# Optimization experiments

Measured on AMD Instinct MI355X. Metric: run time of the kernel, lower is better.

The kernel has to match this reference:

```python
import jax, jax.numpy as jnp
import numpy as np

N, E = 50000, 800000
IN_F, EDGE_F = 512, 32
HEADS, HID = 4, 64  # per-layer: H*C = 256
NEG_SLOPE = 0.2


def _gatv2_layer(x, src, dst, edge_attr, Wl, bl, Wr, br, We, att, bias):
    # PyG GATv2Conv: x_l = lin_l(x) (used as message value), x_r = lin_r(x)
    n = x.shape[0]
    H, C = att.shape
    xl = (x @ Wl + bl).reshape(n, H, C)
    xr = (x @ Wr + br).reshape(n, H, C)
    ea = (edge_attr @ We).reshape(-1, H, C)          # lin_edge (no bias)
    m = jax.nn.leaky_relu(xl[src] + xr[dst] + ea, NEG_SLOPE)  # [E,H,C]
    logits = jnp.einsum('ehc,hc->eh', m, att)        # [E,H]
    # segment softmax over incoming edges of each destination node
    mx = jax.ops.segment_max(logits, dst, num_segments=n)
    ex = jnp.exp(logits - mx[dst])
    denom = jax.ops.segment_sum(ex, dst, num_segments=n)
    alpha = ex / denom[dst]                          # [E,H]
    out = jax.ops.segment_sum(alpha[:, :, None] * xl[src], dst, num_segments=n)
    return out.reshape(n, H * C) + bias


def setup_inputs() -> dict:
    key = jax.random.key(0)
    ks = jax.random.split(key, 16)
    s = lambda fan_in: 1.0 / np.sqrt(fan_in)
    inp = {
        'x': jax.random.normal(ks[0], (N, IN_F), jnp.float32),
        'edge_index': jax.random.randint(ks[1], (2, E), 0, N, jnp.int64),
        'edge_attr': jax.random.normal(ks[2], (E, EDGE_F), jnp.float32),
        'W_l0': jax.random.normal(ks[3], (IN_F, HEADS * HID), jnp.float32) * s(IN_F),
        'b_l0': jnp.zeros((HEADS * HID,), jnp.float32),
        'W_r0': jax.random.normal(ks[4], (IN_F, HEADS * HID), jnp.float32) * s(IN_F),
        'b_r0': jnp.zeros((HEADS * HID,), jnp.float32),
        'W_e0': jax.random.normal(ks[5], (EDGE_F, HEADS * HID), jnp.float32) * s(EDGE_F),
        'att0': jax.random.normal(ks[6], (HEADS, HID), jnp.float32) * s(HID),
        'bias0': jnp.zeros((HEADS * HID,), jnp.float32),
        'W_l1': jax.random.normal(ks[7], (HEADS * HID, HEADS * HID), jnp.float32) * s(HEADS * HID),
        'b_l1': jnp.zeros((HEADS * HID,), jnp.float32),
        'W_r1': jax.random.normal(ks[8], (HEADS * HID, HEADS * HID), jnp.float32) * s(HEADS * HID),
        'b_r1': jnp.zeros((HEADS * HID,), jnp.float32),
        'W_e1': jax.random.normal(ks[9], (EDGE_F, HEADS * HID), jnp.float32) * s(EDGE_F),
        'att1': jax.random.normal(ks[10], (HEADS, HID), jnp.float32) * s(HID),
        'bias1': jnp.zeros((HEADS * HID,), jnp.float32),
        'W_out': jax.random.normal(ks[11], (HEADS * HID, 1), jnp.float32) * s(HEADS * HID),
        'b_out': jnp.zeros((1,), jnp.float32),
    }
    return inp


def reference(x, edge_index, edge_attr,
              W_l0, b_l0, W_r0, b_r0, W_e0, att0, bias0,
              W_l1, b_l1, W_r1, b_r1, W_e1, att1, bias1,
              W_out, b_out):
    src, dst = edge_index[0], edge_index[1]
    h = jax.nn.relu(_gatv2_layer(x, src, dst, edge_attr, W_l0, b_l0, W_r0, b_r0, W_e0, att0, bias0))
    h = jax.nn.relu(_gatv2_layer(h, src, dst, edge_attr, W_l1, b_l1, W_r1, b_r1, W_e1, att1, bias1))
    return h @ W_out + b_out
```

## Files before the change

kernel.cpp:

```cpp
#include <hip/hip_runtime.h>
#include <hip/hip_bf16.h>

#define NEG_SLOPE 0.2f

typedef __attribute__((ext_vector_type(8))) short bf16x8;
typedef __attribute__((ext_vector_type(4))) float f32x4;

__device__ __forceinline__ unsigned short bf16hi(float v) {
    __hip_bfloat16 h = __float2bfloat16(v);
    return *(unsigned short*)&h;
}
__device__ __forceinline__ float bf16tof(unsigned short u) {
    __hip_bfloat16 h = *(__hip_bfloat16*)&u;
    return __bfloat162float(h);
}

__global__ void hist_kernel(const int* __restrict__ dst, int* __restrict__ cnt, int E) {
    int e = blockIdx.x * 256 + threadIdx.x;
    if (e < E) atomicAdd(&cnt[dst[e]], 1);
}

__global__ void scan_s1(const int* __restrict__ cnt, int* __restrict__ excl,
                        int* __restrict__ totals, int N) {
    __shared__ int lds[256];
    int t = threadIdx.x;
    int i = blockIdx.x * 256 + t;
    int v = (i < N) ? cnt[i] : 0;
    lds[t] = v;
    __syncthreads();
    #pragma unroll
    for (int off = 1; off < 256; off <<= 1) {
        int add = (t >= off) ? lds[t - off] : 0;
        __syncthreads();
        lds[t] += add;
        __syncthreads();
    }
    if (i < N) excl[i] = lds[t] - v;
    if (t == 255) totals[blockIdx.x] = lds[255];
}

__global__ void scan_s2(int* __restrict__ totals, int nb) {
    __shared__ int lds[256];
    int t = threadIdx.x;
    int v = (t < nb) ? totals[t] : 0;
    lds[t] = v;
    __syncthreads();
    #pragma unroll
    for (int off = 1; off < 256; off <<= 1) {
        int add = (t >= off) ? lds[t - off] : 0;
        __syncthreads();
        lds[t] += add;
        __syncthreads();
    }
    if (t < nb) totals[t] = lds[t] - v;
}

__global__ void scan_s3(int* __restrict__ row_ptr, const int* __restrict__ totals,
                        int* __restrict__ cursor, int N, int E) {
    int i = blockIdx.x * 256 + threadIdx.x;
    if (i < N) {
        int v = row_ptr[i] + totals[blockIdx.x];
        row_ptr[i] = v;
        cursor[i] = v;
    }
    if (i == 0) row_ptr[N] = E;
}

__global__ void scatter_kernel(const int* __restrict__ src, const int* __restrict__ dst,
                               int* __restrict__ cursor, int* __restrict__ col_src,
                               int* __restrict__ col_dst, int* __restrict__ col_eid, int E) {
    int e = blockIdx.x * 256 + threadIdx.x;
    if (e < E) {
        int d = dst[e];
        int pos = atomicAdd(&cursor[d], 1);
        col_src[pos] = src[e];
        col_dst[pos] = d;
        col_eid[pos] = e;
    }
}

__global__ void pack_we(const float* __restrict__ We0, const float* __restrict__ We1,
                        unsigned short* __restrict__ WeP) {
    int t = blockIdx.x * 256 + threadIdx.x;
    if (t >= 4096) return;
    int layer = t >> 11;
    int part  = (t >> 10) & 1;
    int tile  = (t >> 6) & 15;
    int lane  = t & 63;
    const float* We = layer ? We1 : We0;
    int ch = tile * 16 + (lane & 15);
    int kb = (lane >> 4) * 8;
    union { unsigned short u[8]; uint4 v; } out;
    #pragma unroll
    for (int j = 0; j < 8; ++j) {
        float w = We[(size_t)(kb + j) * 256 + ch];
        unsigned short hi = bf16hi(w);
        out.u[j] = part ? bf16hi(w - bf16tof(hi)) : hi;
    }
    *(uint4*)(WeP + (size_t)t * 8) = out.v;
}

__global__ void pack_w(const float* __restrict__ Wl, const float* __restrict__ Wr,
                       int KT, unsigned short* __restrict__ out) {
    int t = blockIdx.x * 256 + threadIdx.x;
    int per = KT * 2048;
    if (t >= 2 * per) return;
    int part = t / per;
    int rem  = t % per;
    int kt   = rem >> 11;
    int nt   = (rem >> 6) & 31;
    int lane = rem & 63;
    int n  = nt * 16 + (lane & 15);
    int kb = kt * 32 + ((lane >> 4) * 8);
    const float* W = (n < 256) ? (Wl + n) : (Wr + (n - 256));
    union { unsigned short u[8]; uint4 v; } o;
    #pragma unroll
    for (int j = 0; j < 8; ++j) {
        float w = W[(size_t)(kb + j) * 256];
        unsigned short hi = bf16hi(w);
        o.u[j] = part ? bf16hi(w - bf16tof(hi)) : hi;
    }
    *(uint4*)(out + (size_t)t * 8) = o.v;
}

__global__ __launch_bounds__(256) void gemm_split(
    const float* __restrict__ A, int M, int K,
    const unsigned short* __restrict__ Bf,
    const float* __restrict__ bl, const float* __restrict__ br,
    float* __restrict__ C)
{
    __shared__ unsigned short Af[2][8][64][8];
    const int tid  = threadIdx.x;
    const int lane = tid & 63;
    const int w    = tid >> 6;
    const int m0   = blockIdx.x * 128;
    const int n0   = blockIdx.y * 128;
    const int KT   = K >> 5;
    const int ntg0 = n0 >> 4;

    f32x4 acc[2][8];
    #pragma unroll
    for (int i = 0; i < 2; ++i)
        #pragma unroll
        for (int j = 0; j < 8; ++j) acc[i][j] = (f32x4){0.f, 0.f, 0.f, 0.f};

    const size_t partStride = (size_t)KT * 32 * 512;

    for (int kt = 0; kt < KT; ++kt) {
        #pragma unroll
        for (int i = 0; i < 4; ++i) {
            int idx = tid * 4 + i;
            int r   = idx >> 3;
            int kl  = (idx & 7) * 4;
            int gm  = m0 + r;
            float4 v = make_float4(0.f, 0.f, 0.f, 0.f);
            if (gm < M) v = *(const float4*)(A + (size_t)gm * K + kt * 32 + kl);
            unsigned short h0 = bf16hi(v.x), h1 = bf16hi(v.y);
            unsigned short h2 = bf16hi(v.z), h3 = bf16hi(v.w);
            unsigned short l0 = bf16hi(v.x - bf16tof(h0));
            unsigned short l1 = bf16hi(v.y - bf16tof(h1));
            unsigned short l2 = bf16hi(v.z - bf16tof(h2));
            unsigned short l3 = bf16hi(v.w - bf16tof(h3));
            int mt = r >> 4;
            int la = (r & 15) | ((kl >> 3) << 4);
            int j0 = kl & 7;
            *(uint2*)&Af[0][mt][la][j0] =
                make_uint2((unsigned int)h0 | ((unsigned int)h1 << 16),
                           (unsigned int)h2 | ((unsigned int)h3 << 16));
            *(uint2*)&Af[1][mt][la][j0] =
                make_uint2((unsigned int)l0 | ((unsigned int)l1 << 16),
                           (unsigned int)l2 | ((unsigned int)l3 << 16));
        }
        __syncthreads();

        bf16x8 ah0 = *(const bf16x8*)&Af[0][w * 2 + 0][lane][0];
        bf16x8 ah1 = *(const bf16x8*)&Af[0][w * 2 + 1][lane][0];
        bf16x8 al0 = *(const bf16x8*)&Af[1][w * 2 + 0][lane][0];
        bf16x8 al1 = *(const bf16x8*)&Af[1][w * 2 + 1][lane][0];

        const unsigned short* bbase =
            Bf + ((size_t)kt * 32 + ntg0) * 512 + (size_t)lane * 8;
        #pragma unroll
        for (int nt = 0; nt < 8; ++nt) {
            bf16x8 bh  = *(const bf16x8*)(bbase + (size_t)nt * 512);
            bf16x8 blv = *(const bf16x8*)(bbase + partStride + (size_t)nt * 512);
            acc[0][nt] = __builtin_amdgcn_mfma_f32_16x16x32_bf16(ah0, bh,  acc[0][nt], 0, 0, 0);
            acc[1][nt] = __builtin_amdgcn_mfma_f32_16x16x32_bf16(ah1, bh,  acc[1][nt], 0, 0, 0);
            acc[0][nt] = __builtin_amdgcn_mfma_f32_16x16x32_bf16(ah0, blv, acc[0][nt], 0, 0, 0);
            acc[1][nt] = __builtin_amdgcn_mfma_f32_16x16x32_bf16(ah1, blv, acc[1][nt], 0, 0, 0);
            acc[0][nt] = __builtin_amdgcn_mfma_f32_16x16x32_bf16(al0, bh,  acc[0][nt], 0, 0, 0);
            acc[1][nt] = __builtin_amdgcn_mfma_f32_16x16x32_bf16(al1, bh,  acc[1][nt], 0, 0, 0);
        }
        __syncthreads();
    }

    const int q  = lane >> 4;
    const int cl = lane & 15;
    #pragma unroll
    for (int mti = 0; mti < 2; ++mti) {
        int gmb = m0 + (w * 2 + mti) * 16 + q * 4;
        #pragma unroll
        for (int nt = 0; nt < 8; ++nt) {
            int col = n0 + nt * 16 + cl;
            float bia = (col < 256) ? bl[col] : br[col - 256];
            #pragma unroll
            for (int r = 0; r < 4; ++r) {
                int gm = gmb + r;
                if (gm < M) C[(size_t)gm * 512 + col] = acc[mti][nt][r] + bia;
            }
        }
    }
}

template<bool PROJ>
__global__ __launch_bounds__(256) void gat_fused_t(
    const float* __restrict__ xlxr,
    const float* __restrict__ edge_attr,
    const int* __restrict__ col_src,
    const int* __restrict__ col_dst,
    const int* __restrict__ col_eid,
    const int* __restrict__ row_ptr,
    const unsigned short* __restrict__ WePl,
    const float* __restrict__ att,
    const float* __restrict__ bias,
    float* __restrict__ nmr,
    const float* __restrict__ Wout,
    const float* __restrict__ bout,
    float* __restrict__ out,
    float* __restrict__ denomB,
    int E, int W)
{
    __shared__ unsigned short AhiS[16][64][8];
    __shared__ unsigned short AloS[16][64][8];
    const int tid = threadIdx.x;
    #pragma unroll
    for (int i = 0; i < 4; ++i) {
        int idx = tid * 4 + i;
        ((uint4*)&AhiS[0][0][0])[idx] = ((const uint4*)WePl)[idx];
        ((uint4*)&AloS[0][0][0])[idx] = ((const uint4*)(WePl + 8192))[idx];
    }
    __syncthreads();

    const int lane  = tid & 63;
    const int wid   = tid >> 6;
    const int q     = lane >> 4;
    const int e_sub = lane & 15;
    const int kb    = q * 8;
    const int ch4   = lane * 4;

    const int gw = blockIdx.x * 4 + wid;
    const int s_range = gw * W;
    if (s_range >= E) return;
    const int eEnd = min(E, s_range + W);

    const float4 bia4 = *(const float4*)(bias + ch4);
    float4 wo4 = make_float4(0.f, 0.f, 0.f, 0.f);
    if (PROJ) wo4 = *(const float4*)(Wout + ch4);

    int curDst = -1;
    float4 accB = make_float4(0.f, 0.f, 0.f, 0.f);
    float denB = 0.f;

    auto flush = [&]() {
        if (curDst >= 0) {
            int ra = row_ptr[curDst], rb = row_ptr[curDst + 1];
            bool comp = (ra % W != 0) && (rb % W != 0) && (ra / W == (rb - 1) / W);
            if (comp) {
                float inv = 1.0f / denB;
                float4 o;
                o.x = fmaxf(fmaf(accB.x, inv, bia4.x), 0.f);
                o.y = fmaxf(fmaf(accB.y, inv, bia4.y), 0.f);
                o.z = fmaxf(fmaf(accB.z, inv, bia4.z), 0.f);
                o.w = fmaxf(fmaf(accB.w, inv, bia4.w), 0.f);
                if (!PROJ) {
                    *(float4*)(nmr + (size_t)curDst * 256 + ch4) = o;
                } else {
                    float s = o.x * wo4.x;
                    s = fmaf(o.y, wo4.y, s);
                    s = fmaf(o.z, wo4.z, s);
                    s = fmaf(o.w, wo4.w, s);
                    #pragma unroll
                    for (int off = 32; off > 0; off >>= 1)
                        s += __shfl_xor(s, off, 64);
                    if (lane == 0) out[curDst] = s + bout[0];
                }
            } else {
                float* np = nmr + (size_t)curDst * 256 + ch4;
                atomicAdd(np + 0, accB.x);
                atomicAdd(np + 1, accB.y);
                atomicAdd(np + 2, accB.z);
                atomicAdd(np + 3, accB.w);
                if (e_sub == 0) atomicAdd(denomB + curDst * 4 + q, denB);
            }
            accB = make_float4(0.f, 0.f, 0.f, 0.f);
            denB = 0.f;
        }
    };

    for (int base = s_range; base < eEnd; base += 16) {
        const int cnt  = min(16, eEnd - base);
        const int slot = base + e_sub;
        const int sc   = min(slot, eEnd - 1);
        const int eid  = col_eid[sc];
        const int srcn = col_src[sc];
        const int dstn = col_dst[sc];

        const float* ap = edge_attr + (size_t)eid * 32 + kb;
        float4 v0 = *(const float4*)ap;
        float4 v1 = *(const float4*)(ap + 4);
        float vv[8] = {v0.x, v0.y, v0.z, v0.w, v1.x, v1.y, v1.z, v1.w};
        union { bf16x8 v; unsigned short u[8]; } bh, bl;
        #pragma unroll
        for (int i = 0; i < 8; ++i) {
            unsigned short hh = bf16hi(vv[i]);
            bh.u[i] = hh;
            bl.u[i] = bf16hi(vv[i] - bf16tof(hh));
        }

        const float* xlp = xlxr + (size_t)srcn * 512 + q * 4;
        const float* xrp = xlxr + (size_t)dstn * 512 + 256 + q * 4;

        float lph[4] = {0.f, 0.f, 0.f, 0.f};
        #pragma unroll
        for (int t = 0; t < 16; ++t) {
            bf16x8 ahi = *(const bf16x8*)&AhiS[t][lane][0];
            bf16x8 alo = *(const bf16x8*)&AloS[t][lane][0];
            f32x4 macc = {0.f, 0.f, 0.f, 0.f};
            macc = __builtin_amdgcn_mfma_f32_16x16x32_bf16(ahi, bh.v, macc, 0, 0, 0);
            macc = __builtin_amdgcn_mfma_f32_16x16x32_bf16(ahi, bl.v, macc, 0, 0, 0);
            macc = __builtin_amdgcn_mfma_f32_16x16x32_bf16(alo, bh.v, macc, 0, 0, 0);
            const float4 xl4 = *(const float4*)(xlp + t * 16);
            const float4 xr4 = *(const float4*)(xrp + t * 16);
            const float4 at4 = *(const float4*)(att + t * 16 + q * 4);
            float z0 = macc[0] + xl4.x + xr4.x; z0 = (z0 > 0.f) ? z0 : NEG_SLOPE * z0;
            float z1 = macc[1] + xl4.y + xr4.y; z1 = (z1 > 0.f) ? z1 : NEG_SLOPE * z1;
            float z2 = macc[2] + xl4.z + xr4.z; z2 = (z2 > 0.f) ? z2 : NEG_SLOPE * z2;
            float z3 = macc[3] + xl4.w + xr4.w; z3 = (z3 > 0.f) ? z3 : NEG_SLOPE * z3;
            float s = z0 * at4.x;
            s = fmaf(z1, at4.y, s);
            s = fmaf(z2, at4.z, s);
            s = fmaf(z3, at4.w, s);
            lph[t >> 2] += s;
        }
        #pragma unroll
        for (int hh = 0; hh < 4; ++hh) {
            lph[hh] += __shfl_xor(lph[hh], 16, 64);
            lph[hh] += __shfl_xor(lph[hh], 32, 64);
        }
        float lsel = (q == 0) ? lph[0] : (q == 1) ? lph[1] : (q == 2) ? lph[2] : lph[3];
        float psrc = __expf(lsel);

        auto phaseB = [&](int cnt2) {
            for (int eb = 0; eb < cnt2; eb += 4) {
                float pv[4]; int sv[4], dv[4];
                #pragma unroll
                for (int i = 0; i < 4; ++i) {
                    int e = eb + i;
                    int ec = (e < cnt2) ? e : cnt2 - 1;
                    pv[i] = __shfl(psrc, (lane & 48) | ec, 64);
                    if (e >= cnt2) pv[i] = 0.f;
                    sv[i] = __shfl(srcn, ec, 64);
                    dv[i] = __shfl(dstn, ec, 64);
                }
                float4 xv[4];
                #pragma unroll
                for (int i = 0; i < 4; ++i)
                    xv[i] = *(const float4*)(xlxr + (size_t)sv[i] * 512 + ch4);
                #pragma unroll
                for (int i = 0; i < 4; ++i) {
                    if (dv[i] != curDst) { flush(); curDst = dv[i]; }
                    denB += pv[i];
                    accB.x = fmaf(pv[i], xv[i].x, accB.x);
                    accB.y = fmaf(pv[i], xv[i].y, accB.y);
                    accB.z = fmaf(pv[i], xv[i].z, accB.z);
                    accB.w = fmaf(pv[i], xv[i].w, accB.w);
                }
            }
        };
        if (cnt == 16) phaseB(16); else phaseB(cnt);
    }
    flush();
}

template<bool PROJ>
__global__ __launch_bounds__(256) void finalize_t(
    const int* __restrict__ row_ptr,
    const float* __restrict__ denomB,
    const float* __restrict__ bias,
    float* __restrict__ nmr,
    const float* __restrict__ Wout, const float* __restrict__ bout,
    float* __restrict__ out, int N, int W)
{
    const int tid  = threadIdx.x;
    const int lane = tid & 63;
    const int wid  = tid >> 6;
    const int n = blockIdx.x * 4 + wid;
    if (n >= N) return;
    const int q   = lane >> 4;
    const int ch4 = lane * 4;

    const int a = row_ptr[n], b = row_ptr[n + 1];
    float4 o;
    if (a == b) {
        const float4 bia = *(const float4*)(bias + ch4);
        o.x = fmaxf(bia.x, 0.f);
        o.y = fmaxf(bia.y, 0.f);
        o.z = fmaxf(bia.z, 0.f);
        o.w = fmaxf(bia.w, 0.f);
    } else {
        bool comp = (a % W != 0) && (b % W != 0) && (a / W == (b - 1) / W);
        if (comp) return;
        const float4 nm = *(const float4*)(nmr + (size_t)n * 256 + ch4);
        const float inv = 1.0f / denomB[n * 4 + q];
        const float4 bia = *(const float4*)(bias + ch4);
        o.x = fmaxf(fmaf(nm.x, inv, bia.x), 0.f);
        o.y = fmaxf(fmaf(nm.y, inv, bia.y), 0.f);
        o.z = fmaxf(fmaf(nm.z, inv, bia.z), 0.f);
        o.w = fmaxf(fmaf(nm.w, inv, bia.w), 0.f);
    }
    if (!PROJ) {
        *(float4*)(nmr + (size_t)n * 256 + ch4) = o;
    } else {
        const float4 w4 = *(const float4*)(Wout + ch4);
        float s = o.x * w4.x;
        s = fmaf(o.y, w4.y, s);
        s = fmaf(o.z, w4.z, s);
        s = fmaf(o.w, w4.w, s);
        #pragma unroll
        for (int off = 32; off > 0; off >>= 1)
            s += __shfl_xor(s, off, 64);
        if (lane == 0) out[n] = s + bout[0];
    }
}

extern "C" void kernel_launch(void* const* d_in, const int* in_sizes, int n_in,
                              void* d_out, int out_size, void* d_ws, size_t ws_size,
                              hipStream_t stream) {
    const float* x         = (const float*)d_in[0];
    const int*   edge_idx  = (const int*)d_in[1];
    const float* edge_attr = (const float*)d_in[2];
    const float* W_l0 = (const float*)d_in[3];
    const float* b_l0 = (const float*)d_in[4];
    const float* W_r0 = (const float*)d_in[5];
    const float* b_r0 = (const float*)d_in[6];
    const float* W_e0 = (const float*)d_in[7];
    const float* att0 = (const float*)d_in[8];
    const float* bias0= (const float*)d_in[9];
    const float* W_l1 = (const float*)d_in[10];
    const float* b_l1 = (const float*)d_in[11];
    const float* W_r1 = (const float*)d_in[12];
    const float* b_r1 = (const float*)d_in[13];
    const float* W_e1 = (const float*)d_in[14];
    const float* att1 = (const float*)d_in[15];
    const float* bias1= (const float*)d_in[16];
    const float* W_out= (const float*)d_in[17];
    const float* b_out= (const float*)d_in[18];

    const int N = in_sizes[0] / 512;
    const int E = in_sizes[1] / 2;

    const int* src = edge_idx;
    const int* dst = edge_idx + E;

    char* ws = (char*)d_ws;
    size_t off = 0;
    float* bufA   = (float*)(ws + off); off += (size_t)N * 512 * 4;
    float* bufB   = (float*)(ws + off); off += (size_t)N * 256 * 4;
    float* denomB = (float*)(ws + off); off += (size_t)N * 4 * 4;
    int* row_ptr  = (int*)(ws + off);   off += (((size_t)(N + 1) * 4 + 255) & ~(size_t)255);
    int* cursor   = (int*)(ws + off);   off += (((size_t)N * 4 + 255) & ~(size_t)255);
    int* col_src  = (int*)(ws + off);   off += (size_t)E * 4;
    int* col_dst  = (int*)(ws + off);   off += (size_t)E * 4;
    int* col_eid  = (int*)(ws + off);   off += (size_t)E * 4;
    int* totals   = (int*)(ws + off);   off += 1024;
    unsigned short* WeP = (unsigned short*)(ws + off); off += 4096 * 8 * 2;
    unsigned short* Bf0 = (unsigned short*)(ws + off); off += (size_t)2 * 16 * 32 * 64 * 8 * 2;
    unsigned short* Bf1 = (unsigned short*)(ws + off); off += (size_t)2 * 8 * 32 * 64 * 8 * 2;

    const int nbE = (E + 255) / 256;
    const int nbN = (N + 255) / 256;

    hipMemsetAsync(cursor, 0, (size_t)N * 4, stream);
    hist_kernel<<<nbE, 256, 0, stream>>>(dst, cursor, E);
    scan_s1<<<nbN, 256, 0, stream>>>(cursor, row_ptr, totals, N);
    scan_s2<<<1, 256, 0, stream>>>(totals, nbN);
    scan_s3<<<nbN, 256, 0, stream>>>(row_ptr, totals, cursor, N, E);
    scatter_kernel<<<nbE, 256, 0, stream>>>(src, dst, cursor, col_src, col_dst, col_eid, E);
    pack_we<<<16, 256, 0, stream>>>(W_e0, W_e1, WeP);
    pack_w<<<256, 256, 0, stream>>>(W_l0, W_r0, 16, Bf0);
    pack_w<<<128, 256, 0, stream>>>(W_l1, W_r1, 8, Bf1);

    dim3 ggrid((N + 127) / 128, 4);

    const int NW  = 8192;
    const int nch = (E + 15) / 16;
    const int C   = (nch + NW - 1) / NW;
    const int W   = C * 16;
    const int nfin = (N + 3) / 4;

    gemm_split<<<ggrid, 256, 0, stream>>>(x, N, 512, Bf0, b_l0, b_r0, bufA);
    hipMemsetAsync(bufB,   0, (size_t)N * 256 * 4, stream);
    hipMemsetAsync(denomB, 0, (size_t)N * 4 * 4,   stream);
    gat_fused_t<false><<<2048, 256, 0, stream>>>(
        bufA, edge_attr, col_src, col_dst, col_eid, row_ptr, WeP, att0, bias0,
        bufB, nullptr, nullptr, nullptr, denomB, E, W);
    finalize_t<false><<<nfin, 256, 0, stream>>>(
        row_ptr, denomB, bias0, bufB, nullptr, nullptr, nullptr, N, W);

    gemm_split<<<ggrid, 256, 0, stream>>>(bufB, N, 256, Bf1, b_l1, b_r1, bufA);
    hipMemsetAsync(bufB,   0, (size_t)N * 256 * 4, stream);
    hipMemsetAsync(denomB, 0, (size_t)N * 4 * 4,   stream);
    gat_fused_t<true><<<2048, 256, 0, stream>>>(
        bufA, edge_attr, col_src, col_dst, col_eid, row_ptr, WeP + 16384, att1, bias1,
        bufB, W_out, b_out, (float*)d_out, denomB, E, W);
    finalize_t<true><<<nfin, 256, 0, stream>>>(
        row_ptr, denomB, bias1, bufB, W_out, b_out, (float*)d_out, N, W);
}
```

Before: 1.131 ms.

## Pre-split activations into packed bf16 hi/lo tiles before GEMM with XCD remap

Adds a conversion pass that splits the fp32 activation matrix into bf16 hi and lo parts and stores them in MFMA-fragment-ordered tiles. The new GEMM then loads A straight into LDS with global_load_lds, so the per-tile fp32-to-bf16 split no longer runs inside the GEMM. Blocks are also remapped so neighbouring tiles land on the same XCD, which should improve L2 reuse. The cost is an extra full read and write of A through the workspace, and the fast path only runs when N is a multiple of 16 and the workspace is large enough.

```diff
diff --git a/kernel.cpp b/kernel.cpp
--- a/kernel.cpp
+++ b/kernel.cpp
@@ -121,6 +121,117 @@
         o.u[j] = part ? bf16hi(w - bf16tof(hi)) : hi;
     }
     *(uint4*)(out + (size_t)t * 8) = o.v;
+}
+
+__global__ __launch_bounds__(256) void conv_a(
+    const float* __restrict__ A, int K, int ntiles,
+    unsigned short* __restrict__ Apk)
+{
+    int gw = (blockIdx.x * 256 + threadIdx.x) >> 6;
+    int lane = threadIdx.x & 63;
+    if (gw >= ntiles) return;
+    int KT  = K >> 5;
+    int mtg = gw / KT;
+    int kt  = gw % KT;
+    int r16 = lane & 15;
+    int kg  = lane >> 4;
+    const float* ap = A + (size_t)(mtg * 16 + r16) * K + kt * 32 + kg * 8;
+    float4 v0 = *(const float4*)ap;
+    float4 v1 = *(const float4*)(ap + 4);
+    float vv[8] = {v0.x, v0.y, v0.z, v0.w, v1.x, v1.y, v1.z, v1.w};
+    union { unsigned short u[8]; uint4 q; } hi, lo;
+    #pragma unroll
+    for (int j = 0; j < 8; ++j) {
+        unsigned short h = bf16hi(vv[j]);
+        hi.u[j] = h;
+        lo.u[j] = bf16hi(vv[j] - bf16tof(h));
+    }
+    size_t tb = (size_t)gw * 1024;
+    *(uint4*)(Apk + tb + lane * 8)       = hi.q;
+    *(uint4*)(Apk + tb + 512 + lane * 8) = lo.q;
+}
+
+__global__ __launch_bounds__(256) void gemm_split2(
+    const unsigned short* __restrict__ Apk, int M, int K,
+    const unsigned short* __restrict__ Bf,
+    const float* __restrict__ bl, const float* __restrict__ br,
+    float* __restrict__ C)
+{
+    __shared__ unsigned short Af[2][8][64][8];
+    const int tid  = threadIdx.x;
+    const int lane = tid & 63;
+    const int w    = tid >> 6;
+
+    const int nwg = gridDim.x;
+    const int q8 = nwg >> 3, r8 = nwg & 7;
+    const int xcd = blockIdx.x & 7, idx = blockIdx.x >> 3;
+    const int L = (xcd < r8) ? xcd * (q8 + 1) + idx
+                             : r8 * (q8 + 1) + (xcd - r8) * q8 + idx;
+    const int m0   = (L >> 2) * 128;
+    const int n0   = (L & 3) * 128;
+    const int KT   = K >> 5;
+    const int ntg0 = n0 >> 4;
+    const int mtg0 = m0 >> 4;
+
+    f32x4 acc[2][8];
+    #pragma unroll
+    for (int i = 0; i < 2; ++i)
+        #pragma unroll
+        for (int j = 0; j < 8; ++j) acc[i][j] = (f32x4){0.f, 0.f, 0.f, 0.f};
+
+    const size_t partStride = (size_t)KT * 32 * 512;
+
+    for (int kt = 0; kt < KT; ++kt) {
+        #pragma unroll
+        for (int ii = 0; ii < 4; ++ii) {
+            int i = w * 4 + ii;
+            int mt = i >> 1, part = i & 1;
+            const unsigned short* g =
+                Apk + ((size_t)((mtg0 + mt) * KT + kt) * 2 + part) * 512 + lane * 8;
+            unsigned short* l = &Af[part][mt][0][0];
+            __builtin_amdgcn_global_load_lds(
+                (const __attribute__((address_space(1))) unsigned int*)g,
+                (__attribute__((address_space(3))) unsigned int*)l, 16, 0, 0);
+        }
+        __syncthreads();
+
+        bf16x8 ah0 = *(const bf16x8*)&Af[0][w * 2 + 0][lane][0];
+        bf16x8 ah1 = *(const bf16x8*)&Af[0][w * 2 + 1][lane][0];
+        bf16x8 al0 = *(const bf16x8*)&Af[1][w * 2 + 0][lane][0];
+        bf16x8 al1 = *(const bf16x8*)&Af[1][w * 2 + 1][lane][0];
+
+        const unsigned short* bbase =
+            Bf + ((size_t)kt * 32 + ntg0) * 512 + (size_t)lane * 8;
+        #pragma unroll
+        for (int nt = 0; nt < 8; ++nt) {
+            bf16x8 bh  = *(const bf16x8*)(bbase + (size_t)nt * 512);
+            bf16x8 blv = *(const bf16x8*)(bbase + partStride + (size_t)nt * 512);
+            acc[0][nt] = __builtin_amdgcn_mfma_f32_16x16x32_bf16(ah0, bh,  acc[0][nt], 0, 0, 0);
+            acc[1][nt] = __builtin_amdgcn_mfma_f32_16x16x32_bf16(ah1, bh,  acc[1][nt], 0, 0, 0);
+            acc[0][nt] = __builtin_amdgcn_mfma_f32_16x16x32_bf16(ah0, blv, acc[0][nt], 0, 0, 0);
+            acc[1][nt] = __builtin_amdgcn_mfma_f32_16x16x32_bf16(ah1, blv, acc[1][nt], 0, 0, 0);
+            acc[0][nt] = __builtin_amdgcn_mfma_f32_16x16x32_bf16(al0, bh,  acc[0][nt], 0, 0, 0);
+            acc[1][nt] = __builtin_amdgcn_mfma_f32_16x16x32_bf16(al1, bh,  acc[1][nt], 0, 0, 0);
+        }
+        __syncthreads();
+    }
+
+    const int q  = lane >> 4;
+    const int cl = lane & 15;
+    #pragma unroll
+    for (int mti = 0; mti < 2; ++mti) {
+        int gmb = m0 + (w * 2 + mti) * 16 + q * 4;
+        #pragma unroll
+        for (int nt = 0; nt < 8; ++nt) {
+            int col = n0 + nt * 16 + cl;
+            float bia = (col < 256) ? bl[col] : br[col - 256];
+            #pragma unroll
+            for (int r = 0; r < 4; ++r) {
+                int gm = gmb + r;
+                if (gm < M) C[(size_t)gm * 512 + col] = acc[mti][nt][r] + bia;
+            }
+        }
+    }
 }
 
 __global__ __launch_bounds__(256) void gemm_split(
@@ -477,6 +588,13 @@
     unsigned short* Bf0 = (unsigned short*)(ws + off); off += (size_t)2 * 16 * 32 * 64 * 8 * 2;
     unsigned short* Bf1 = (unsigned short*)(ws + off); off += (size_t)2 * 8 * 32 * 64 * 8 * 2;
 
+    const int ntiles0 = (N >> 4) * 16;
+    const int ntiles1 = (N >> 4) * 8;
+    unsigned short* Apk = (unsigned short*)(ws + off);
+    size_t apkBytes = (size_t)(ntiles0 > ntiles1 ? ntiles0 : ntiles1) * 2048 + 131072;
+    off += apkBytes;
+    const bool fast = (off <= ws_size) && ((N & 15) == 0);
+
     const int nbE = (E + 255) / 256;
     const int nbN = (N + 255) / 256;
 
@@ -490,7 +608,8 @@
     pack_w<<<256, 256, 0, stream>>>(W_l0, W_r0, 16, Bf0);
     pack_w<<<128, 256, 0, stream>>>(W_l1, W_r1, 8, Bf1);
 
-    dim3 ggrid((N + 127) / 128, 4);
+    const int nbx = (N + 127) / 128;
+    dim3 ggrid(nbx, 4);
 
     const int NW  = 8192;
     const int nch = (E + 15) / 16;
@@ -498,7 +617,12 @@
     const int W   = C * 16;
     const int nfin = (N + 3) / 4;
 
-    gemm_split<<<ggrid, 256, 0, stream>>>(x, N, 512, Bf0, b_l0, b_r0, bufA);
+    if (fast) {
+        conv_a<<<(ntiles0 + 3) / 4, 256, 0, stream>>>(x, 512, ntiles0, Apk);
+        gemm_split2<<<nbx * 4, 256, 0, stream>>>(Apk, N, 512, Bf0, b_l0, b_r0, bufA);
+    } else {
+        gemm_split<<<ggrid, 256, 0, stream>>>(x, N, 512, Bf0, b_l0, b_r0, bufA);
+    }
     hipMemsetAsync(bufB,   0, (size_t)N * 256 * 4, stream);
     hipMemsetAsync(denomB, 0, (size_t)N * 4 * 4,   stream);
     gat_fused_t<false><<<2048, 256, 0, stream>>>(
@@ -507,7 +631,12 @@
     finalize_t<false><<<nfin, 256, 0, stream>>>(
         row_ptr, denomB, bias0, bufB, nullptr, nullptr, nullptr, N, W);
 
-    gemm_split<<<ggrid, 256, 0, stream>>>(bufB, N, 256, Bf1, b_l1, b_r1, bufA);
+    if (fast) {
+        conv_a<<<(ntiles1 + 3) / 4, 256, 0, stream>>>(bufB, 256, ntiles1, Apk);
+        gemm_split2<<<nbx * 4, 256, 0, stream>>>(Apk, N, 256, Bf1, b_l1, b_r1, bufA);
+    } else {
+        gemm_split<<<ggrid, 256, 0, stream>>>(bufB, N, 256, Bf1, b_l1, b_r1, bufA);
+    }
     hipMemsetAsync(bufB,   0, (size_t)N * 256 * 4, stream);
     hipMemsetAsync(denomB, 0, (size_t)N * 4 * 4,   stream);
     gat_fused_t<true><<<2048, 256, 0, stream>>>(
```

After: 1.145 ms. No clear change (+1.2%).
